# Performance work log

Hardware: AMD Instinct MI355X
Metric: run time of the kernel (lower is better)

The kernel has to match this reference:

```python
import jax, jax.numpy as jnp
import numpy as np

N_GRID = 65160   # 181*360 lat-lon grid nodes (= self.size)
N_MESH = 40962   # level-6 icosphere nodes
N_TOT = N_GRID + N_MESH
E = 521280
IN_CH = 96
HID = 256
OUT_CH = 96


def setup_inputs() -> dict:
    key = jax.random.key(0)
    ks = jax.random.split(key, 12)
    inp = {
        'x': jax.random.normal(ks[0], (1, IN_CH, N_MESH), jnp.float32),
        'x_res_grid': jax.random.normal(ks[1], (1, IN_CH, N_GRID), jnp.float32),
        'edge_index': jax.random.randint(ks[2], (2, E), 0, N_TOT, jnp.int64),
        # GCNConv 1 (in_ch -> 256), glorot-ish scale
        'W1': jax.random.normal(ks[3], (IN_CH, HID), jnp.float32) * (2.0 / (IN_CH + HID)) ** 0.5,
        'b1': jnp.zeros((HID,), jnp.float32),
        # GCNConv 2 (256 -> 256)
        'W2': jax.random.normal(ks[4], (HID, HID), jnp.float32) * (2.0 / (HID + HID)) ** 0.5,
        'b2': jnp.zeros((HID,), jnp.float32),
        # Lmodel2: Linear(256,256) -> Linear(256,out_ch), xavier_normal
        'Wl1': jax.random.normal(ks[5], (HID, HID), jnp.float32) * (2.0 / (HID + HID)) ** 0.5,
        'bl1': jnp.zeros((HID,), jnp.float32),
        'Wl2': jax.random.normal(ks[6], (HID, OUT_CH), jnp.float32) * (2.0 / (HID + OUT_CH)) ** 0.5,
        'bl2': jnp.zeros((OUT_CH,), jnp.float32),
    }
    return inp


def _gcn_norm(edge_index, n_nodes):
    # PyG gcn_norm with add_self_loops=True, edge_weight=1
    loop = jnp.arange(n_nodes, dtype=edge_index.dtype)
    src = jnp.concatenate([edge_index[0], loop])
    dst = jnp.concatenate([edge_index[1], loop])
    deg = jnp.zeros((n_nodes,), jnp.float32).at[dst].add(1.0)
    dinv = jnp.where(deg > 0, jax.lax.rsqrt(deg), 0.0)
    norm = dinv[src] * dinv[dst]  # [E+N]
    return src, dst, norm


def _gcn_conv(h, W, b, src, dst, norm):
    # h: [B, N, C] -> [B, N, H]; x' = D^-1/2 (A+I) D^-1/2 (h W) + b
    m = h @ W                                   # [B, N, H]
    msg = m[:, src, :] * norm[None, :, None]    # [B, E+N, H]
    agg = jnp.zeros(m.shape, m.dtype).at[:, dst].add(msg)
    return agg + b


def reference(x, x_res_grid, edge_index, W1, b1, W2, b2, Wl1, bl1, Wl2, bl2):
    nodes = jnp.concatenate([x_res_grid, x], axis=-1)  # [B, C, N]
    h = nodes.transpose(0, 2, 1)                       # [B, N, C]
    n = h.shape[1]
    src, dst, norm = _gcn_norm(edge_index, n)
    h = _gcn_conv(h, W1, b1, src, dst, norm)
    h = jax.nn.gelu(h, approximate=False)              # torch nn.GELU (exact erf)
    h = _gcn_conv(h, W2, b2, src, dst, norm)           # [B, N, 256]
    g = h[:, :N_GRID, :]                               # slice grid nodes
    out = (g @ Wl1 + bl1) @ Wl2 + bl2                  # [B, size, out_ch]
    return out.transpose(0, 2, 1)                      # [B, out_ch, size]
```

## Files before the change

kernel.cpp:

```cpp
#include <hip/hip_runtime.h>
#include <math.h>

#define N_GRID 65160
#define N_MESH 40962
#define N_TOT  106122
#define NE     521280
#define IN_CH  96
#define HID    256
#define OUT_CH 96

typedef __attribute__((ext_vector_type(8))) short bf16x8;
typedef __attribute__((ext_vector_type(4))) float f32x4;

__device__ __forceinline__ unsigned short f2bf(float f) {
  unsigned u = __float_as_uint(f);
  return (unsigned short)((u + 0x7FFFu + ((u >> 16) & 1u)) >> 16);
}
__device__ __forceinline__ float bf2f(unsigned short s) {
  return __uint_as_float(((unsigned)s) << 16);
}
__device__ __forceinline__ void unp8(uint4 v, float* f) {
  f[0] = __uint_as_float(v.x << 16); f[1] = __uint_as_float(v.x & 0xFFFF0000u);
  f[2] = __uint_as_float(v.y << 16); f[3] = __uint_as_float(v.y & 0xFFFF0000u);
  f[4] = __uint_as_float(v.z << 16); f[5] = __uint_as_float(v.z & 0xFFFF0000u);
  f[6] = __uint_as_float(v.w << 16); f[7] = __uint_as_float(v.w & 0xFFFF0000u);
}

__global__ void k_concat_transpose(const float* __restrict__ xg, const float* __restrict__ xm,
                                   unsigned short* __restrict__ h) {
  __shared__ float tile[IN_CH][65];
  int base = blockIdx.x * 64;
  int t = threadIdx.x;
#pragma unroll
  for (int it = 0; it < 24; ++it) {
    int lin = t + it * 256;
    int c  = lin >> 6;
    int n0 = lin & 63;
    int n = base + n0;
    float v = 0.f;
    if (n < N_TOT) {
      v = (n < N_GRID) ? xg[(size_t)c * N_GRID + n]
                       : xm[(size_t)c * N_MESH + (n - N_GRID)];
    }
    tile[c][n0] = v;
  }
  __syncthreads();
#pragma unroll
  for (int it = 0; it < 24; ++it) {
    int lin = t + it * 256;
    int c  = lin % 96;
    int n0 = lin / 96;
    int n = base + n0;
    if (n < N_TOT) h[(size_t)n * IN_CH + c] = f2bf(tile[c][n0]);
  }
}

__global__ void k_transpose_out(const float* __restrict__ tb, float* __restrict__ out) {
  __shared__ float tile[IN_CH][65];
  int base = blockIdx.x * 64;
  int t = threadIdx.x;
#pragma unroll
  for (int it = 0; it < 24; ++it) {
    int lin = t + it * 256;
    int c  = lin % 96;
    int n0 = lin / 96;
    int n = base + n0;
    if (n < N_GRID) tile[c][n0] = tb[(size_t)n * 96 + c];
  }
  __syncthreads();
#pragma unroll
  for (int it = 0; it < 24; ++it) {
    int lin = t + it * 256;
    int c  = lin >> 6;
    int n0 = lin & 63;
    int n = base + n0;
    if (n < N_GRID) out[(size_t)c * N_GRID + n] = tile[c][n0];
  }
}

__global__ void k_zeroi(int* __restrict__ p, int n) {
  int i = blockIdx.x * 256 + threadIdx.x;
  if (i < n) p[i] = 0;
}

__global__ void k_hist(const int* __restrict__ dst, int* __restrict__ deg) {
  int e = blockIdx.x * 256 + threadIdx.x;
  if (e < NE) atomicAdd(&deg[dst[e]], 1);
}

__global__ void k_blocksum(const int* __restrict__ deg, int* __restrict__ bsum, int n) {
  __shared__ int s[256];
  int i = blockIdx.x * 256 + threadIdx.x;
  s[threadIdx.x] = (i < n) ? deg[i] : 0;
  __syncthreads();
  for (int st = 128; st > 0; st >>= 1) {
    if (threadIdx.x < st) s[threadIdx.x] += s[threadIdx.x + st];
    __syncthreads();
  }
  if (threadIdx.x == 0) bsum[blockIdx.x] = s[0];
}

__global__ void k_scanbsum(int* __restrict__ bsum, int nb) {
  __shared__ int s[512];
  int t = threadIdx.x;
  int v = (t < nb) ? bsum[t] : 0;
  s[t] = v;
  __syncthreads();
  for (int off = 1; off < 512; off <<= 1) {
    int x = (t >= off) ? s[t - off] : 0;
    __syncthreads();
    s[t] += x;
    __syncthreads();
  }
  if (t < nb) bsum[t] = s[t] - v;
}

__global__ void k_offsets(const int* __restrict__ deg, const int* __restrict__ bsum,
                          int* __restrict__ off, int* __restrict__ cur,
                          float* __restrict__ dinv, int n) {
  __shared__ int s[256];
  int i = blockIdx.x * 256 + threadIdx.x;
  int v = (i < n) ? deg[i] : 0;
  s[threadIdx.x] = v;
  __syncthreads();
  for (int o = 1; o < 256; o <<= 1) {
    int x = (threadIdx.x >= o) ? s[threadIdx.x - o] : 0;
    __syncthreads();
    s[threadIdx.x] += x;
    __syncthreads();
  }
  if (i < n) {
    int e = bsum[blockIdx.x] + s[threadIdx.x] - v;
    off[i] = e;
    cur[i] = e;
    dinv[i] = rsqrtf(1.0f + (float)v);
  }
  if (i == 0) off[n] = NE;
}

__global__ void k_fillcsr(const int* __restrict__ src, const int* __restrict__ dst,
                          int* __restrict__ cur, int* __restrict__ csrc) {
  int e = blockIdx.x * 256 + threadIdx.x;
  if (e < NE) {
    int p = atomicAdd(&cur[dst[e]], 1);
    csrc[p] = src[e];
  }
}

__global__ void k_gather96(const int* __restrict__ off, const int* __restrict__ csrc,
                           const float* __restrict__ dinv, const unsigned short* __restrict__ h,
                           unsigned short* __restrict__ agg) {
  int i = blockIdx.x * 256 + threadIdx.x;
  if (i >= N_TOT * 12) return;
  int n = i / 12;
  int c8 = (i % 12) << 3;
  float di = dinv[n];
  float acc[8], f[8];
  uint4 v = *(const uint4*)(h + (size_t)n * 96 + c8);
  unp8(v, f);
  float w0 = di * di;
#pragma unroll
  for (int j = 0; j < 8; ++j) acc[j] = f[j] * w0;
  int e0 = off[n], e1 = off[n + 1];
  int e = e0;
  for (; e + 3 < e1; e += 4) {
    int s0 = csrc[e], s1 = csrc[e + 1], s2 = csrc[e + 2], s3 = csrc[e + 3];
    float wa = dinv[s0] * di, wb = dinv[s1] * di, wc = dinv[s2] * di, wd = dinv[s3] * di;
    uint4 u0 = *(const uint4*)(h + (size_t)s0 * 96 + c8);
    uint4 u1 = *(const uint4*)(h + (size_t)s1 * 96 + c8);
    uint4 u2 = *(const uint4*)(h + (size_t)s2 * 96 + c8);
    uint4 u3 = *(const uint4*)(h + (size_t)s3 * 96 + c8);
    float g0[8], g1[8], g2[8], g3[8];
    unp8(u0, g0); unp8(u1, g1); unp8(u2, g2); unp8(u3, g3);
#pragma unroll
    for (int j = 0; j < 8; ++j) acc[j] += g0[j] * wa + g1[j] * wb + g2[j] * wc + g3[j] * wd;
  }
  for (; e < e1; ++e) {
    int s = csrc[e];
    float w = dinv[s] * di;
    uint4 u = *(const uint4*)(h + (size_t)s * 96 + c8);
    unp8(u, f);
#pragma unroll
    for (int j = 0; j < 8; ++j) acc[j] += f[j] * w;
  }
  uint4 o;
  o.x = (unsigned)f2bf(acc[0]) | ((unsigned)f2bf(acc[1]) << 16);
  o.y = (unsigned)f2bf(acc[2]) | ((unsigned)f2bf(acc[3]) << 16);
  o.z = (unsigned)f2bf(acc[4]) | ((unsigned)f2bf(acc[5]) << 16);
  o.w = (unsigned)f2bf(acc[6]) | ((unsigned)f2bf(acc[7]) << 16);
  *(uint4*)(agg + (size_t)n * 96 + c8) = o;
}

__global__ void k_gather96p(const int* __restrict__ off, const int* __restrict__ csrc,
                            const float* __restrict__ dinv, const unsigned short* __restrict__ p,
                            const float* __restrict__ bc, float* __restrict__ tb) {
  int i = blockIdx.x * 256 + threadIdx.x;
  if (i >= N_GRID * 12) return;
  int n = i / 12;
  int c8 = (i % 12) << 3;
  float di = dinv[n];
  float acc[8], f[8];
  uint4 v = *(const uint4*)(p + (size_t)n * 96 + c8);
  unp8(v, f);
  float w0 = di * di;
#pragma unroll
  for (int j = 0; j < 8; ++j) acc[j] = f[j] * w0;
  int e0 = off[n], e1 = off[n + 1];
  int e = e0;
  for (; e + 3 < e1; e += 4) {
    int s0 = csrc[e], s1 = csrc[e + 1], s2 = csrc[e + 2], s3 = csrc[e + 3];
    float wa = dinv[s0] * di, wb = dinv[s1] * di, wc = dinv[s2] * di, wd = dinv[s3] * di;
    uint4 u0 = *(const uint4*)(p + (size_t)s0 * 96 + c8);
    uint4 u1 = *(const uint4*)(p + (size_t)s1 * 96 + c8);
    uint4 u2 = *(const uint4*)(p + (size_t)s2 * 96 + c8);
    uint4 u3 = *(const uint4*)(p + (size_t)s3 * 96 + c8);
    float g0[8], g1[8], g2[8], g3[8];
    unp8(u0, g0); unp8(u1, g1); unp8(u2, g2); unp8(u3, g3);
#pragma unroll
    for (int j = 0; j < 8; ++j) acc[j] += g0[j] * wa + g1[j] * wb + g2[j] * wc + g3[j] * wd;
  }
  for (; e < e1; ++e) {
    int s = csrc[e];
    float w = dinv[s] * di;
    uint4 u = *(const uint4*)(p + (size_t)s * 96 + c8);
    unp8(u, f);
#pragma unroll
    for (int j = 0; j < 8; ++j) acc[j] += f[j] * w;
  }
  float* row = tb + (size_t)n * 96 + c8;
  *(float4*)(row)     = make_float4(acc[0] + bc[c8 + 0], acc[1] + bc[c8 + 1],
                                    acc[2] + bc[c8 + 2], acc[3] + bc[c8 + 3]);
  *(float4*)(row + 4) = make_float4(acc[4] + bc[c8 + 4], acc[5] + bc[c8 + 5],
                                    acc[6] + bc[c8 + 6], acc[7] + bc[c8 + 7]);
}

__global__ __launch_bounds__(256, 2) void k_wgemm96(const float* __restrict__ A, const float* __restrict__ bvec,
                                                    const float* __restrict__ B, float* __restrict__ C,
                                                    int M, int K) {
  __shared__ float As[64][33];
  __shared__ float Bs[64][100];
  int t = threadIdx.x;
  int tx = t & 15, ty = t >> 4;
  int bm = blockIdx.x * 32;
  float acc[2][6] = {};
  for (int kc = 0; kc < K; kc += 64) {
#pragma unroll
    for (int it = 0; it < 2; ++it) {
      int idx = t + it * 256;
      int r = idx >> 4, k4 = (idx & 15) << 2;
      int gr = bm + r;
      float4 v = make_float4(0.f, 0.f, 0.f, 0.f);
      if (gr < M) {
        const float* src = (gr < M - 1) ? (A + (size_t)gr * K + kc + k4) : (bvec + kc + k4);
        v = *(const float4*)src;
      }
      As[k4 + 0][r] = v.x;
      As[k4 + 1][r] = v.y;
      As[k4 + 2][r] = v.z;
      As[k4 + 3][r] = v.w;
    }
#pragma unroll
    for (int it = 0; it < 6; ++it) {
      int idx = t + it * 256;
      int k = idx / 24, j4 = (idx % 24) << 2;
      float4 v = *(const float4*)(B + (size_t)(kc + k) * 96 + j4);
      *(float4*)&Bs[k][j4] = v;
    }
    __syncthreads();
#pragma unroll
    for (int k = 0; k < 64; ++k) {
      float a0 = As[k][ty * 2], a1 = As[k][ty * 2 + 1];
      float w[6];
      *(float2*)&w[0] = *(const float2*)&Bs[k][tx * 6];
      *(float2*)&w[2] = *(const float2*)&Bs[k][tx * 6 + 2];
      *(float2*)&w[4] = *(const float2*)&Bs[k][tx * 6 + 4];
#pragma unroll
      for (int j = 0; j < 6; ++j) { acc[0][j] += a0 * w[j]; acc[1][j] += a1 * w[j]; }
    }
    __syncthreads();
  }
#pragma unroll
  for (int i = 0; i < 2; ++i) {
    int gr = bm + ty * 2 + i;
    if (gr >= M) continue;
    float* row = C + (size_t)gr * 96 + tx * 6;
    row[0] = acc[i][0]; row[1] = acc[i][1]; row[2] = acc[i][2];
    row[3] = acc[i][3]; row[4] = acc[i][4]; row[5] = acc[i][5];
  }
}

__global__ void k_cast_w1t(const float* __restrict__ W1, unsigned short* __restrict__ W1bt) {
  int idx = blockIdx.x * 256 + threadIdx.x;
  if (idx >= 256 * 96) return;
  int n = idx / 96, k = idx % 96;
  W1bt[idx] = f2bf(W1[(size_t)k * 256 + n]);
}
__global__ void k_cast_wct(const float* __restrict__ P2, const float* __restrict__ r1,
                           const float* __restrict__ bl2, unsigned short* __restrict__ Wcbt,
                           float* __restrict__ bc) {
  int idx = blockIdx.x * 256 + threadIdx.x;
  if (blockIdx.x == 0 && threadIdx.x < OUT_CH)
    bc[threadIdx.x] = r1[threadIdx.x] + P2[256 * 96 + threadIdx.x] + bl2[threadIdx.x];
  if (idx >= 96 * 256) return;
  int n = idx / 256, k = idx % 256;
  Wcbt[idx] = f2bf(P2[(size_t)k * 96 + n]);
}

#define SWZ(row, g) (((row) << 7) + (((g) ^ ((row) & 7)) << 3))
__global__ __launch_bounds__(256, 4) void k_mlp(const unsigned short* __restrict__ A,
                                                const unsigned short* __restrict__ W1bt,
                                                const float* __restrict__ bias1,
                                                const unsigned short* __restrict__ Wcbt,
                                                unsigned short* __restrict__ P, int M) {
  __shared__ unsigned short Hs[64 * 128];
  __shared__ unsigned short Ws[64 * 128];
  int t = threadIdx.x;
  int wave = t >> 6, lane = t & 63;
  int l15 = lane & 15, lhi = lane >> 4;
  int bm = blockIdx.x * 64;

  int arowl = wave * 16 + l15;
  bool aok = (bm + arowl) < M;
  const unsigned short* ap = A + (size_t)(bm + arowl) * 96 + lhi * 8;
  bf16x8 a0 = aok ? *(const bf16x8*)(ap)      : (bf16x8){0,0,0,0,0,0,0,0};
  bf16x8 a1 = aok ? *(const bf16x8*)(ap + 32) : (bf16x8){0,0,0,0,0,0,0,0};
  bf16x8 a2 = aok ? *(const bf16x8*)(ap + 64) : (bf16x8){0,0,0,0,0,0,0,0};
  int hrow = wave * 16 + lhi * 4;
  int orow = wave * 16 + lhi * 4;

  f32x4 accC[6];
#pragma unroll
  for (int q = 0; q < 6; ++q) accC[q] = (f32x4){0.f, 0.f, 0.f, 0.f};

  for (int hf = 0; hf < 2; ++hf) {
    for (int c = 0; c < 2; ++c) {
      __syncthreads();
#pragma unroll
      for (int it = 0; it < 3; ++it) {
        int idx = t + it * 256;
        int row = idx / 12, g = idx % 12;
        *(uint4*)&Ws[SWZ(row, g)] =
            *(const uint4*)(W1bt + (size_t)(hf * 128 + c * 64 + row) * 96 + g * 8);
      }
      __syncthreads();
#pragma unroll
      for (int fl = 0; fl < 4; ++fl) {
        int floc = c * 4 + fl;
        int wrow = fl * 16 + l15;
        bf16x8 w0_ = *(const bf16x8*)&Ws[SWZ(wrow, 0 + lhi)];
        bf16x8 w1_ = *(const bf16x8*)&Ws[SWZ(wrow, 4 + lhi)];
        bf16x8 w2_ = *(const bf16x8*)&Ws[SWZ(wrow, 8 + lhi)];
        f32x4 acc = (f32x4){0.f, 0.f, 0.f, 0.f};
        acc = __builtin_amdgcn_mfma_f32_16x16x32_bf16(a0, w0_, acc, 0, 0, 0);
        acc = __builtin_amdgcn_mfma_f32_16x16x32_bf16(a1, w1_, acc, 0, 0, 0);
        acc = __builtin_amdgcn_mfma_f32_16x16x32_bf16(a2, w2_, acc, 0, 0, 0);
        int col = (hf * 8 + floc) * 16 + l15;
        int colh = floc * 16 + l15;
        float bv = bias1[col];
#pragma unroll
        for (int r = 0; r < 4; ++r) {
          float x = acc[r] + bv;
          x = 0.5f * x * (1.0f + erff(x * 0.70710678118654752f));
          int row = hrow + r;
          Hs[SWZ(row, colh >> 3) + (colh & 7)] = f2bf(x);
        }
      }
    }

    for (int tf = 0; tf < 2; ++tf) {
      __syncthreads();
#pragma unroll
      for (int it = 0; it < 3; ++it) {
        int idx = t + it * 256;
        int row = idx >> 4, g = idx & 15;
        *(uint4*)&Ws[SWZ(row, g)] =
            *(const uint4*)(Wcbt + (size_t)(tf * 48 + row) * 256 + hf * 128 + g * 8);
      }
      __syncthreads();
#pragma unroll
      for (int fl = 0; fl < 3; ++fl) {
        int wrow = fl * 16 + l15;
        int harow = wave * 16 + l15;
#pragma unroll
        for (int ks = 0; ks < 4; ++ks) {
          bf16x8 av = *(const bf16x8*)&Hs[SWZ(harow, ks * 4 + lhi)];
          bf16x8 wv = *(const bf16x8*)&Ws[SWZ(wrow, ks * 4 + lhi)];
          accC[tf * 3 + fl] = __builtin_amdgcn_mfma_f32_16x16x32_bf16(av, wv, accC[tf * 3 + fl], 0, 0, 0);
        }
      }
    }
  }

#pragma unroll
  for (int q = 0; q < 6; ++q) {
    int col = (q / 3) * 48 + (q % 3) * 16 + l15;
#pragma unroll
    for (int r = 0; r < 4; ++r) {
      int row = bm + orow + r;
      if (row < M) P[(size_t)row * 96 + col] = f2bf(accC[q][r]);
    }
  }
}

extern "C" void kernel_launch(void* const* d_in, const int* in_sizes, int n_in,
                              void* d_out, int out_size, void* d_ws, size_t ws_size,
                              hipStream_t stream) {
  const float* xm  = (const float*)d_in[0];
  const float* xg  = (const float*)d_in[1];
  const int*   ei  = (const int*)d_in[2];
  const float* W1  = (const float*)d_in[3];
  const float* b1  = (const float*)d_in[4];
  const float* W2  = (const float*)d_in[5];
  const float* b2  = (const float*)d_in[6];
  const float* Wl1 = (const float*)d_in[7];
  const float* bl1 = (const float*)d_in[8];
  const float* Wl2 = (const float*)d_in[9];
  const float* bl2 = (const float*)d_in[10];
  float* out = (float*)d_out;

  float* W0 = (float*)d_ws;
  const size_t MB = (size_t)N_GRID * 256;
  int*   deg  = (int*)(W0 + MB);
  int*   off  = deg + N_TOT;
  int*   cur  = off + N_TOT + 1;
  int*   bsum = cur + N_TOT;
  int*   csrc = bsum + 512;
  float* dinv = (float*)(csrc + NE);
  size_t p1off = ((size_t)(dinv + N_TOT - W0) + 3) & ~(size_t)3;
  float* P1 = W0 + p1off;
  float* P2 = P1 + 257 * 96;
  float* bc = P2 + 257 * 96;
  size_t wboff = ((size_t)(bc + 96 - W0) + 3) & ~(size_t)3;
  unsigned short* W1bt = (unsigned short*)(W0 + wboff);
  unsigned short* Wcbt = W1bt + 256 * 96;
  size_t RH = (wboff + 24576 + 3) & ~(size_t)3;
  unsigned short* hb = (unsigned short*)(W0 + RH);
  unsigned short* agg1b = (unsigned short*)W0;
  unsigned short* p = (unsigned short*)(hb + (size_t)N_TOT * 96 + 16);
  p = (unsigned short*)(((size_t)p + 15) & ~(size_t)15);
  float* tb = W0 + (size_t)6 * 1024 * 1024;

  const int* esrc = ei;
  const int* edst = ei + NE;
  dim3 b256(256);
  const int NB_N = (N_TOT + 255) / 256;

  k_concat_transpose<<<dim3((N_TOT + 63) / 64), b256, 0, stream>>>(xg, xm, hb);

  k_zeroi<<<dim3(NB_N), b256, 0, stream>>>(deg, N_TOT);
  k_hist<<<dim3((NE + 255) / 256), b256, 0, stream>>>(edst, deg);
  k_blocksum<<<dim3(NB_N), b256, 0, stream>>>(deg, bsum, N_TOT);
  k_scanbsum<<<dim3(1), dim3(512), 0, stream>>>(bsum, NB_N);
  k_offsets<<<dim3(NB_N), b256, 0, stream>>>(deg, bsum, off, cur, dinv, N_TOT);
  k_fillcsr<<<dim3((NE + 255) / 256), b256, 0, stream>>>(esrc, edst, cur, csrc);
  k_cast_w1t<<<dim3(96), b256, 0, stream>>>(W1, W1bt);
  k_wgemm96<<<dim3(9), b256, 0, stream>>>(Wl1, bl1, Wl2, P1, 257, HID);
  k_wgemm96<<<dim3(9), b256, 0, stream>>>(W2, b2, P1, P2, 257, HID);
  k_cast_wct<<<dim3(96), b256, 0, stream>>>(P2, P1 + 256 * 96, bl2, Wcbt, bc);

  k_gather96<<<dim3((N_TOT * 12 + 255) / 256), b256, 0, stream>>>(off, csrc, dinv, hb, agg1b);

  k_mlp<<<dim3((N_TOT + 63) / 64), b256, 0, stream>>>(agg1b, W1bt, b1, Wcbt, p, N_TOT);

  k_gather96p<<<dim3((N_GRID * 12 + 255) / 256), b256, 0, stream>>>(off, csrc, dinv, p, bc, tb);

  k_transpose_out<<<dim3((N_GRID + 63) / 64), b256, 0, stream>>>(tb, out);
}
```

Baseline: 222.8 us.

## Fuse final gather with output transpose and replace zero kernel with memset

The second-layer gather over grid nodes now writes its results straight into a shared-memory tile, which is then written out transposed. This removes the fp32 intermediate buffer and the separate transpose kernel, along with that buffer's global write and re-read. The degree-zeroing kernel is also replaced by hipMemsetAsync. The fused kernel uses 64-node blocks with 3 tasks per thread, which gives fewer, larger blocks and may reduce latency hiding during the irregular gather.

```diff
diff --git a/kernel.cpp b/kernel.cpp
--- a/kernel.cpp
+++ b/kernel.cpp
@@ -53,34 +53,6 @@
     int n = base + n0;
     if (n < N_TOT) h[(size_t)n * IN_CH + c] = f2bf(tile[c][n0]);
   }
-}
-
-__global__ void k_transpose_out(const float* __restrict__ tb, float* __restrict__ out) {
-  __shared__ float tile[IN_CH][65];
-  int base = blockIdx.x * 64;
-  int t = threadIdx.x;
-#pragma unroll
-  for (int it = 0; it < 24; ++it) {
-    int lin = t + it * 256;
-    int c  = lin % 96;
-    int n0 = lin / 96;
-    int n = base + n0;
-    if (n < N_GRID) tile[c][n0] = tb[(size_t)n * 96 + c];
-  }
-  __syncthreads();
-#pragma unroll
-  for (int it = 0; it < 24; ++it) {
-    int lin = t + it * 256;
-    int c  = lin >> 6;
-    int n0 = lin & 63;
-    int n = base + n0;
-    if (n < N_GRID) out[(size_t)c * N_GRID + n] = tile[c][n0];
-  }
-}
-
-__global__ void k_zeroi(int* __restrict__ p, int n) {
-  int i = blockIdx.x * 256 + threadIdx.x;
-  if (i < n) p[i] = 0;
 }
 
 __global__ void k_hist(const int* __restrict__ dst, int* __restrict__ deg) {
@@ -191,47 +163,61 @@
   *(uint4*)(agg + (size_t)n * 96 + c8) = o;
 }
 
-__global__ void k_gather96p(const int* __restrict__ off, const int* __restrict__ csrc,
-                            const float* __restrict__ dinv, const unsigned short* __restrict__ p,
-                            const float* __restrict__ bc, float* __restrict__ tb) {
-  int i = blockIdx.x * 256 + threadIdx.x;
-  if (i >= N_GRID * 12) return;
-  int n = i / 12;
-  int c8 = (i % 12) << 3;
-  float di = dinv[n];
-  float acc[8], f[8];
-  uint4 v = *(const uint4*)(p + (size_t)n * 96 + c8);
-  unp8(v, f);
-  float w0 = di * di;
-#pragma unroll
-  for (int j = 0; j < 8; ++j) acc[j] = f[j] * w0;
-  int e0 = off[n], e1 = off[n + 1];
-  int e = e0;
-  for (; e + 3 < e1; e += 4) {
-    int s0 = csrc[e], s1 = csrc[e + 1], s2 = csrc[e + 2], s3 = csrc[e + 3];
-    float wa = dinv[s0] * di, wb = dinv[s1] * di, wc = dinv[s2] * di, wd = dinv[s3] * di;
-    uint4 u0 = *(const uint4*)(p + (size_t)s0 * 96 + c8);
-    uint4 u1 = *(const uint4*)(p + (size_t)s1 * 96 + c8);
-    uint4 u2 = *(const uint4*)(p + (size_t)s2 * 96 + c8);
-    uint4 u3 = *(const uint4*)(p + (size_t)s3 * 96 + c8);
-    float g0[8], g1[8], g2[8], g3[8];
-    unp8(u0, g0); unp8(u1, g1); unp8(u2, g2); unp8(u3, g3);
-#pragma unroll
-    for (int j = 0; j < 8; ++j) acc[j] += g0[j] * wa + g1[j] * wb + g2[j] * wc + g3[j] * wd;
-  }
-  for (; e < e1; ++e) {
-    int s = csrc[e];
-    float w = dinv[s] * di;
-    uint4 u = *(const uint4*)(p + (size_t)s * 96 + c8);
-    unp8(u, f);
-#pragma unroll
-    for (int j = 0; j < 8; ++j) acc[j] += f[j] * w;
-  }
-  float* row = tb + (size_t)n * 96 + c8;
-  *(float4*)(row)     = make_float4(acc[0] + bc[c8 + 0], acc[1] + bc[c8 + 1],
-                                    acc[2] + bc[c8 + 2], acc[3] + bc[c8 + 3]);
-  *(float4*)(row + 4) = make_float4(acc[4] + bc[c8 + 4], acc[5] + bc[c8 + 5],
-                                    acc[6] + bc[c8 + 6], acc[7] + bc[c8 + 7]);
+__global__ void k_gather_out(const int* __restrict__ off, const int* __restrict__ csrc,
+                             const float* __restrict__ dinv, const unsigned short* __restrict__ p,
+                             const float* __restrict__ bc, float* __restrict__ out) {
+  __shared__ float tile[IN_CH][65];
+  int base = blockIdx.x * 64;
+  int t = threadIdx.x;
+#pragma unroll
+  for (int it = 0; it < 3; ++it) {
+    int task = t + it * 256;
+    int n0 = task / 12;
+    int c8 = (task % 12) << 3;
+    int n = base + n0;
+    if (n < N_GRID) {
+      float di = dinv[n];
+      float acc[8], f[8];
+      uint4 v = *(const uint4*)(p + (size_t)n * 96 + c8);
+      unp8(v, f);
+      float w0 = di * di;
+#pragma unroll
+      for (int j = 0; j < 8; ++j) acc[j] = f[j] * w0;
+      int e0 = off[n], e1 = off[n + 1];
+      int e = e0;
+      for (; e + 3 < e1; e += 4) {
+        int s0 = csrc[e], s1 = csrc[e + 1], s2 = csrc[e + 2], s3 = csrc[e + 3];
+        float wa = dinv[s0] * di, wb = dinv[s1] * di, wc = dinv[s2] * di, wd = dinv[s3] * di;
+        uint4 u0 = *(const uint4*)(p + (size_t)s0 * 96 + c8);
+        uint4 u1 = *(const uint4*)(p + (size_t)s1 * 96 + c8);
+        uint4 u2 = *(const uint4*)(p + (size_t)s2 * 96 + c8);
+        uint4 u3 = *(const uint4*)(p + (size_t)s3 * 96 + c8);
+        float g0[8], g1[8], g2[8], g3[8];
+        unp8(u0, g0); unp8(u1, g1); unp8(u2, g2); unp8(u3, g3);
+#pragma unroll
+        for (int j = 0; j < 8; ++j) acc[j] += g0[j] * wa + g1[j] * wb + g2[j] * wc + g3[j] * wd;
+      }
+      for (; e < e1; ++e) {
+        int s = csrc[e];
+        float w = dinv[s] * di;
+        uint4 u = *(const uint4*)(p + (size_t)s * 96 + c8);
+        unp8(u, f);
+#pragma unroll
+        for (int j = 0; j < 8; ++j) acc[j] += f[j] * w;
+      }
+#pragma unroll
+      for (int j = 0; j < 8; ++j) tile[c8 + j][n0] = acc[j] + bc[c8 + j];
+    }
+  }
+  __syncthreads();
+#pragma unroll
+  for (int it = 0; it < 24; ++it) {
+    int lin = t + it * 256;
+    int c  = lin >> 6;
+    int n0 = lin & 63;
+    int n = base + n0;
+    if (n < N_GRID) out[(size_t)c * N_GRID + n] = tile[c][n0];
+  }
 }
 
 __global__ __launch_bounds__(256, 2) void k_wgemm96(const float* __restrict__ A, const float* __restrict__ bvec,
@@ -366,7 +352,6 @@
         }
       }
     }
-
     for (int tf = 0; tf < 2; ++tf) {
       __syncthreads();
 #pragma unroll
@@ -438,7 +423,6 @@
   unsigned short* agg1b = (unsigned short*)W0;
   unsigned short* p = (unsigned short*)(hb + (size_t)N_TOT * 96 + 16);
   p = (unsigned short*)(((size_t)p + 15) & ~(size_t)15);
-  float* tb = W0 + (size_t)6 * 1024 * 1024;
 
   const int* esrc = ei;
   const int* edst = ei + NE;
@@ -447,7 +431,7 @@
 
   k_concat_transpose<<<dim3((N_TOT + 63) / 64), b256, 0, stream>>>(xg, xm, hb);
 
-  k_zeroi<<<dim3(NB_N), b256, 0, stream>>>(deg, N_TOT);
+  hipMemsetAsync(deg, 0, (size_t)N_TOT * sizeof(int), stream);
   k_hist<<<dim3((NE + 255) / 256), b256, 0, stream>>>(edst, deg);
   k_blocksum<<<dim3(NB_N), b256, 0, stream>>>(deg, bsum, N_TOT);
   k_scanbsum<<<dim3(1), dim3(512), 0, stream>>>(bsum, NB_N);
@@ -462,7 +446,5 @@
 
   k_mlp<<<dim3((N_TOT + 63) / 64), b256, 0, stream>>>(agg1b, W1bt, b1, Wcbt, p, N_TOT);
 
-  k_gather96p<<<dim3((N_GRID * 12 + 255) / 256), b256, 0, stream>>>(off, csrc, dinv, p, bc, tb);
-
-  k_transpose_out<<<dim3((N_GRID + 63) / 64), b256, 0, stream>>>(tb, out);
-}
+  k_gather_out<<<dim3((N_GRID + 63) / 64), b256, 0, stream>>>(off, csrc, dinv, p, bc, out);
+}
```

Measured after the change: 213.2 us. 1.04x faster.
